# Optimization experiments

Hardware: AMD Instinct MI355X
Metric: run time of the kernel (lower is better)

Reference implementation:

```python
import jax, jax.numpy as jnp
import numpy as np

EPSILON = 0.1
N_ITERS = 5
SCALE = 0.05  # keeps exp(-cdist/epsilon) from underflowing to 0


def setup_inputs() -> dict:
    key = jax.random.key(0)
    k1, k2 = jax.random.split(key)
    P = jax.random.normal(k1, (8192, 64), dtype=jnp.float32) * SCALE
    Q = jax.random.normal(k2, (8192, 64), dtype=jnp.float32) * SCALE
    return {"P": P, "Q": Q}


def _cdist(P, Q):
    # Euclidean pairwise distances via the mm expansion (like torch.cdist p=2)
    sq = (jnp.sum(P * P, axis=-1)[:, None]
          + jnp.sum(Q * Q, axis=-1)[None, :]
          - 2.0 * P @ Q.T)
    return jnp.sqrt(jnp.maximum(sq, 0.0))


def reference(P, Q):
    C = _cdist(P, Q)                      # [N, N]
    K = jnp.exp(-C / EPSILON)             # [N, N]
    D = P.shape[1]
    u = jnp.ones((P.shape[0],), dtype=P.dtype) / D
    for _ in range(N_ITERS):              # small fixed iteration count
        v = 1.0 / (K @ u)                 # [N]
        u = 1.0 / (K @ v)                 # [N]
    plan = u[:, None] * K * v[None, :]    # [N, N]
    return jnp.sum(plan * C)
```

## Files before the change

kernel.cpp:

```cpp
#include <hip/hip_runtime.h>
#include <hip/hip_fp16.h>
#include <stdint.h>

#define NROWS 8192
#define DIM 64
#define EPS 0.1f

typedef float f32x4 __attribute__((ext_vector_type(4)));
typedef short s16x8 __attribute__((ext_vector_type(8)));
typedef _Float16 h2 __attribute__((ext_vector_type(2)));


__device__ __forceinline__ float wave_reduce_add(float v) {
  #pragma unroll
  for (int off = 32; off > 0; off >>= 1) v += __shfl_down(v, off, 64);
  return v;
}

__device__ __forceinline__ uint32_t pack_bf16_trunc(float x, float y) {
  return __builtin_amdgcn_perm(__float_as_uint(y), __float_as_uint(x), 0x07060302u);
}

__device__ __forceinline__ int pi_idx(int i) {
  int r = i & 63;
  int tj = r >> 4, quad = (r >> 2) & 3, e = r & 3;
  return (i & ~63) | (quad * 16 + tj * 4 + e);
}


#if __has_builtin(__builtin_amdgcn_cvt_scalef32_pk_f16_fp4)
#define CVT4H(kd, sel) __builtin_amdgcn_cvt_scalef32_pk_f16_fp4((kd), 1.0f, (sel))
#else
__device__ __forceinline__ h2 cvt4h_fb(uint32_t kd, int sel) {
  uint32_t byt  = (kd >> (sel * 8)) & 0xFFu;
  uint32_t selv = (byt & 0xFu) | ((byt >> 4) << 16);
  uint32_t tb = __builtin_amdgcn_perm(0x46444240u, 0x3E3C3800u, selv);
  uint32_t d  = ((tb & 0xFFu) << 8) | ((tb & 0xFF0000u) << 8);
  return __builtin_bit_cast(h2, d);
}
#define CVT4H(kd, sel) cvt4h_fb((kd), (sel))
#endif

#if __has_builtin(__builtin_amdgcn_cvt_scalef32_pk_fp4_f32)
__device__ __forceinline__ uint32_t enc4(float q0, float q1, float q2, float q3) {
  uint32_t pk = __builtin_amdgcn_cvt_scalef32_pk_fp4_f32(0u, q0, q1, 1.0f, 0);
  pk = __builtin_amdgcn_cvt_scalef32_pk_fp4_f32(pk, q2, q3, 1.0f, 1);
  return pk & 0xFFFFu;
}
#else
__device__ __forceinline__ uint32_t enc1(float q) {
  float c = fminf(floorf(2.f * q + 0.5f), 4.f);
  c += (q > 2.5f) ? 1.f : 0.f;
  c += (q > 3.5f) ? 1.f : 0.f;
  return (uint32_t)c;
}
__device__ __forceinline__ uint32_t enc4(float q0, float q1, float q2, float q3) {
  return enc1(q0) | (enc1(q1) << 4) | (enc1(q2) << 8) | (enc1(q3) << 12);
}
#endif

#if __has_builtin(__builtin_amdgcn_exp2f)
#define EXPD(d) __builtin_amdgcn_exp2f(-14.4269504089f * (d))
#else
#define EXPD(d) __expf(-10.0f * (d))
#endif

#define FP4DOT(kd, xv, acc)                                                          \
  acc = __builtin_amdgcn_fdot2(CVT4H((kd), 0), __builtin_bit_cast(h2, (xv).x), acc, false); \
  acc = __builtin_amdgcn_fdot2(CVT4H((kd), 1), __builtin_bit_cast(h2, (xv).y), acc, false); \
  acc = __builtin_amdgcn_fdot2(CVT4H((kd), 2), __builtin_bit_cast(h2, (xv).z), acc, false); \
  acc = __builtin_amdgcn_fdot2(CVT4H((kd), 3), __builtin_bit_cast(h2, (xv).w), acc, false);

#define FIN1(kd, xd_, sel)                                                           \
  {                                                                                  \
    uint32_t byt  = ((kd) >> ((sel) * 8)) & 0xFFu;                                   \
    uint32_t selv = (byt & 0xFu) | ((byt & 0xF0u) << 12);                            \
    uint32_t hi = __builtin_amdgcn_perm(0x4945423Du, 0x3800B500u, selv);             \
    uint32_t lo = __builtin_amdgcn_perm(0x608C978Cu, 0xDE008C00u, selv);             \
    h2 lut = __builtin_bit_cast(h2, lo | (hi << 8));                                 \
    h2 xp  = __builtin_bit_cast(h2, (xd_));                                          \
    s1b = __builtin_amdgcn_fdot2(CVT4H((kd), (sel)), xp, s1b, false);                \
    t2b = __builtin_amdgcn_fdot2(lut, xp, t2b, false);                               \
  }
#define FINDOT(kd, xv) FIN1(kd, (xv).x, 0) FIN1(kd, (xv).y, 1) FIN1(kd, (xv).z, 2) FIN1(kd, (xv).w, 3)


__global__ __launch_bounds__(256) void rownorm_pack(
    const float* __restrict__ P, const float* __restrict__ Q,
    float* __restrict__ p2, float* __restrict__ q2,
    unsigned short* __restrict__ Pb, unsigned short* __restrict__ Qb) {
  int g = blockIdx.x * 256 + threadIdx.x;
  int row = g >> 3, sub = g & 7;
  const float* X;
  float* out;
  unsigned short* Xb;
  int r;
  float sc;
  if (row < NROWS) { X = P; out = p2; Xb = Pb; r = row; sc = -2.f; }
  else             { X = Q; out = q2; Xb = Qb; r = row - NROWS; sc = 1.f; }
  const float4* X4 = (const float4*)(X + (size_t)r * DIM);
  float4 a0 = X4[sub * 2], a1 = X4[sub * 2 + 1];
  float ss = a0.x * a0.x + a0.y * a0.y + a0.z * a0.z + a0.w * a0.w
           + a1.x * a1.x + a1.y * a1.y + a1.z * a1.z + a1.w * a1.w;
  ss += __shfl_xor(ss, 1, 64);
  ss += __shfl_xor(ss, 2, 64);
  ss += __shfl_xor(ss, 4, 64);
  if (sub == 0) out[r] = ss;
  uint4 pk;
  pk.x = pack_bf16_trunc(sc * a0.x, sc * a0.y);
  pk.y = pack_bf16_trunc(sc * a0.z, sc * a0.w);
  pk.z = pack_bf16_trunc(sc * a1.x, sc * a1.y);
  pk.w = pack_bf16_trunc(sc * a1.z, sc * a1.w);
  *(uint4*)(Xb + (size_t)r * DIM + sub * 8) = pk;
}


struct KgenSmem {
  unsigned char A[128 * 128];
  unsigned char B[256 * 128];
};

__device__ __forceinline__ int swiz_off(int row, int kc) {
  return row * 128 + ((kc ^ (row & 7)) << 4);
}

__global__ __launch_bounds__(512) void kgen_kernel(
    const unsigned short* __restrict__ Pb, const unsigned short* __restrict__ Qb,
    const float* __restrict__ p2, const float* __restrict__ q2,
    unsigned char* __restrict__ K4, unsigned char* __restrict__ scales,
    float* __restrict__ rspart) {
  __shared__ KgenSmem sm;
  const int t  = threadIdx.x;
  const int bi = blockIdx.y * 128;
  const int bj = blockIdx.x * 256;

  {
    const uint4* Pb4 = (const uint4*)(Pb + (size_t)bi * DIM);
    const uint4* Qb4 = (const uint4*)(Qb + (size_t)bj * DIM);
    #pragma unroll
    for (int it = 0; it < 2; ++it) {
      int idx = t + it * 512;
      int row = idx >> 3, kc = idx & 7;
      *(uint4*)(sm.A + swiz_off(row, kc)) = Pb4[row * 8 + kc];
    }
    #pragma unroll
    for (int it = 0; it < 4; ++it) {
      int idx = t + it * 512;
      int row = idx >> 3, kc = idx & 7;
      *(uint4*)(sm.B + swiz_off(row, kc)) = Qb4[row * 8 + kc];
    }
  }
  __syncthreads();

  const int w        = t >> 6;
  const int lane     = t & 63;
  const int quad     = lane >> 4;
  const int m16      = lane & 15;
  const int wave_row = (w >> 2) * 64;
  const int wave_col = (w & 3) * 64;

  float pn[4];
  f32x4 qn[4];
  #pragma unroll
  for (int ti = 0; ti < 4; ++ti) pn[ti] = p2[bi + wave_row + ti * 16 + m16];
  #pragma unroll
  for (int tj = 0; tj < 4; ++tj)
    qn[tj] = *(const f32x4*)&q2[bj + wave_col + tj * 16 + quad * 4];

  f32x4 acc[4][4];
  #pragma unroll
  for (int ti = 0; ti < 4; ++ti)
    #pragma unroll
    for (int tj = 0; tj < 4; ++tj) acc[ti][tj] = qn[tj] + pn[ti];

  #pragma unroll
  for (int kstep = 0; kstep < 2; ++kstep) {
    const int kc = kstep * 4 + quad;
    s16x8 af[4], bf[4];
    #pragma unroll
    for (int ti = 0; ti < 4; ++ti)
      af[ti] = *(const s16x8*)(sm.A + swiz_off(wave_row + ti * 16 + m16, kc));
    #pragma unroll
    for (int tj = 0; tj < 4; ++tj)
      bf[tj] = *(const s16x8*)(sm.B + swiz_off(wave_col + tj * 16 + m16, kc));
    #pragma unroll
    for (int ti = 0; ti < 4; ++ti)
      #pragma unroll
      for (int tj = 0; tj < 4; ++tj)
        acc[ti][tj] = __builtin_amdgcn_mfma_f32_16x16x32_bf16(
            bf[tj], af[ti], acc[ti][tj], 0, 0, 0);
  }

  #pragma unroll
  for (int ti = 0; ti < 4; ++ti) {
    const int row = bi + wave_row + ti * 16 + m16;
    float kv[4][4];
    float mx = 0.f, rs = 0.f;
    #pragma unroll
    for (int tj = 0; tj < 4; ++tj) {
      f32x4 sq = acc[ti][tj];
      kv[tj][0] = EXPD(__builtin_amdgcn_sqrtf(fmaxf(sq.x, 0.f)));
      kv[tj][1] = EXPD(__builtin_amdgcn_sqrtf(fmaxf(sq.y, 0.f)));
      kv[tj][2] = EXPD(__builtin_amdgcn_sqrtf(fmaxf(sq.z, 0.f)));
      kv[tj][3] = EXPD(__builtin_amdgcn_sqrtf(fmaxf(sq.w, 0.f)));
      float mt = fmaxf(fmaxf(kv[tj][0], kv[tj][1]), fmaxf(kv[tj][2], kv[tj][3]));
      mx = fmaxf(mx, mt);
      rs += (kv[tj][0] + kv[tj][1]) + (kv[tj][2] + kv[tj][3]);
    }
    mx = fmaxf(mx, __shfl_xor(mx, 16, 64));
    uint32_t eb = (__float_as_uint(mx) >> 23) - 1u;
    float si = __uint_as_float((254u - eb) << 23);
    uint32_t pk0 = enc4(kv[0][0] * si, kv[0][1] * si, kv[0][2] * si, kv[0][3] * si);
    uint32_t pk1 = enc4(kv[1][0] * si, kv[1][1] * si, kv[1][2] * si, kv[1][3] * si);
    uint32_t pk2 = enc4(kv[2][0] * si, kv[2][1] * si, kv[2][2] * si, kv[2][3] * si);
    uint32_t pk3 = enc4(kv[3][0] * si, kv[3][1] * si, kv[3][2] * si, kv[3][3] * si);
    uint2 st = uint2{pk0 | (pk1 << 16), pk2 | (pk3 << 16)};
    *(uint2*)(K4 + (size_t)row * (NROWS / 2) + ((bj + wave_col) >> 1) + quad * 8) = st;
    uint32_t eb2 = (uint32_t)__shfl_xor((int)eb, 32, 64);
    if (quad == 0) {
      *(unsigned short*)(scales + (size_t)row * 256 + ((bj + wave_col) >> 5)) =
          (unsigned short)((eb & 0xFFu) | ((eb2 & 0xFFu) << 8));
    }
    float v = rs;
    v += __shfl_xor(v, 16, 64);
    v += __shfl_xor(v, 32, 64);
    if (quad == 0)
      rspart[(size_t)(blockIdx.x * 4 + (w & 3)) * NROWS + row] = v;
  }
}

__global__ __launch_bounds__(128) void v1_kernel(const float* __restrict__ rspart,
                                                 unsigned short* __restrict__ vb16) {
  int i = blockIdx.x * 128 + threadIdx.x;
  float s = 0.f;
  #pragma unroll 8
  for (int c = 0; c < 128; ++c) s += rspart[(size_t)c * NROWS + i];
  vb16[pi_idx(i)] = __half_as_ushort(__float2half(64.0f / s));
}


__global__ __launch_bounds__(256) void matvec_fp4(
    const unsigned char* __restrict__ K4, const unsigned char* __restrict__ scales,
    const unsigned short* __restrict__ xin, unsigned short* __restrict__ yout) {
  const int t = threadIdx.x, lane = t & 63, w = t >> 6;
  const int p = w >> 1, h = w & 1;
  const int r0 = blockIdx.x * 4 + p * 2;
  const uint4* krow0 = (const uint4*)(K4 + (size_t)r0 * (NROWS / 2));
  const uint4* krow1 = (const uint4*)(K4 + (size_t)(r0 + 1) * (NROWS / 2));
  const unsigned char* srow0 = scales + (size_t)r0 * 256;
  const unsigned char* srow1 = srow0 + 256;
  const uint4* x4 = (const uint4*)xin;
  const int b0 = h * 128 + lane;
  const int b1 = b0 + 64;

  uint4 xa0 = x4[b0 * 4 + 0], xb0 = x4[b0 * 4 + 1];
  uint4 xc0 = x4[b0 * 4 + 2], xd0 = x4[b0 * 4 + 3];
  uint4 xa1 = x4[b1 * 4 + 0], xb1 = x4[b1 * 4 + 1];
  uint4 xc1 = x4[b1 * 4 + 2], xd1 = x4[b1 * 4 + 3];
  uint4 k00 = krow0[b0], k01 = krow0[b1];
  uint4 k10 = krow1[b0], k11 = krow1[b1];
  float S00 = __uint_as_float((uint32_t)srow0[b0] << 23);
  float S01 = __uint_as_float((uint32_t)srow0[b1] << 23);
  float S10 = __uint_as_float((uint32_t)srow1[b0] << 23);
  float S11 = __uint_as_float((uint32_t)srow1[b1] << 23);

  float a0 = 0.f, a1 = 0.f;
  FP4DOT(k00.x, xa0, a0) FP4DOT(k00.y, xb0, a1)
  FP4DOT(k00.z, xc0, a0) FP4DOT(k00.w, xd0, a1)
  float t0 = S00 * (a0 + a1);
  a0 = 0.f; a1 = 0.f;
  FP4DOT(k01.x, xa1, a0) FP4DOT(k01.y, xb1, a1)
  FP4DOT(k01.z, xc1, a0) FP4DOT(k01.w, xd1, a1)
  t0 = fmaf(S01, a0 + a1, t0);
  a0 = 0.f; a1 = 0.f;
  FP4DOT(k10.x, xa0, a0) FP4DOT(k10.y, xb0, a1)
  FP4DOT(k10.z, xc0, a0) FP4DOT(k10.w, xd0, a1)
  float t1 = S10 * (a0 + a1);
  a0 = 0.f; a1 = 0.f;
  FP4DOT(k11.x, xa1, a0) FP4DOT(k11.y, xb1, a1)
  FP4DOT(k11.z, xc1, a0) FP4DOT(k11.w, xd1, a1)
  t1 = fmaf(S11, a0 + a1, t1);

  t0 = wave_reduce_add(t0);
  t1 = wave_reduce_add(t1);
  __shared__ float sred[4][2];
  if (lane == 0) { sred[w][0] = t0; sred[w][1] = t1; }
  __syncthreads();
  if (t < 4) {
    int pp = t >> 1, j = t & 1;
    float tot = sred[pp * 2 + 0][j] + sred[pp * 2 + 1][j];
    yout[pi_idx(blockIdx.x * 4 + pp * 2 + j)] =
        __half_as_ushort(__float2half(1.0f / tot));
  }
}

__global__ __launch_bounds__(256) void final_fp4(
    const unsigned char* __restrict__ K4, const unsigned char* __restrict__ scales,
    const unsigned short* __restrict__ xin, float* __restrict__ partials) {
  const int t = threadIdx.x, lane = t & 63, w = t >> 6;
  const int p = w >> 1, h = w & 1;
  const int r0 = blockIdx.x * 4 + p * 2;
  const uint4* krow0 = (const uint4*)(K4 + (size_t)r0 * (NROWS / 2));
  const uint4* krow1 = (const uint4*)(K4 + (size_t)(r0 + 1) * (NROWS / 2));
  const unsigned char* srow0 = scales + (size_t)r0 * 256;
  const unsigned char* srow1 = srow0 + 256;
  const uint4* x4 = (const uint4*)xin;
  const int b0 = h * 128 + lane;
  const int b1 = b0 + 64;

  uint4 xa0 = x4[b0 * 4 + 0], xb0 = x4[b0 * 4 + 1];
  uint4 xc0 = x4[b0 * 4 + 2], xd0 = x4[b0 * 4 + 3];
  uint4 xa1 = x4[b1 * 4 + 0], xb1 = x4[b1 * 4 + 1];
  uint4 xc1 = x4[b1 * 4 + 2], xd1 = x4[b1 * 4 + 3];
  uint4 k00 = krow0[b0], k01 = krow0[b1];
  uint4 k10 = krow1[b0], k11 = krow1[b1];
  uint32_t sb00 = srow0[b0], sb01 = srow0[b1];
  uint32_t sb10 = srow1[b0], sb11 = srow1[b1];

  float s1_0, s2_0, s1_1, s2_1;
  {
    float S = __uint_as_float(sb00 << 23);
    float lnS = ((float)(int)sb00 - 127.f) * 0.69314718f;
    float s1b = 0.f, t2b = 0.f;
    FINDOT(k00.x, xa0) FINDOT(k00.y, xb0) FINDOT(k00.z, xc0) FINDOT(k00.w, xd0)
    s1_0 = S * s1b;
    s2_0 = S * fmaf(lnS, s1b, t2b);
  }
  {
    float S = __uint_as_float(sb01 << 23);
    float lnS = ((float)(int)sb01 - 127.f) * 0.69314718f;
    float s1b = 0.f, t2b = 0.f;
    FINDOT(k01.x, xa1) FINDOT(k01.y, xb1) FINDOT(k01.z, xc1) FINDOT(k01.w, xd1)
    s1_0 = fmaf(S, s1b, s1_0);
    s2_0 = fmaf(S, fmaf(lnS, s1b, t2b), s2_0);
  }
  {
    float S = __uint_as_float(sb10 << 23);
    float lnS = ((float)(int)sb10 - 127.f) * 0.69314718f;
    float s1b = 0.f, t2b = 0.f;
    FINDOT(k10.x, xa0) FINDOT(k10.y, xb0) FINDOT(k10.z, xc0) FINDOT(k10.w, xd0)
    s1_1 = S * s1b;
    s2_1 = S * fmaf(lnS, s1b, t2b);
  }
  {
    float S = __uint_as_float(sb11 << 23);
    float lnS = ((float)(int)sb11 - 127.f) * 0.69314718f;
    float s1b = 0.f, t2b = 0.f;
    FINDOT(k11.x, xa1) FINDOT(k11.y, xb1) FINDOT(k11.z, xc1) FINDOT(k11.w, xd1)
    s1_1 = fmaf(S, s1b, s1_1);
    s2_1 = fmaf(S, fmaf(lnS, s1b, t2b), s2_1);
  }

  s1_0 = wave_reduce_add(s1_0);
  s2_0 = wave_reduce_add(s2_0);
  s1_1 = wave_reduce_add(s1_1);
  s2_1 = wave_reduce_add(s2_1);
  __shared__ float sred[4][4];
  if (lane == 0) {
    sred[w][0] = s1_0; sred[w][1] = s2_0; sred[w][2] = s1_1; sred[w][3] = s2_1;
  }
  __syncthreads();
  if (t == 0) {
    float acc = 0.f;
    #pragma unroll
    for (int pp = 0; pp < 2; ++pp)
      #pragma unroll
      for (int j = 0; j < 2; ++j) {
        float s1 = sred[pp * 2 + 0][j * 2 + 0] + sred[pp * 2 + 1][j * 2 + 0];
        float s2 = sred[pp * 2 + 0][j * 2 + 1] + sred[pp * 2 + 1][j * 2 + 1];
        acc += s2 / s1;
      }
    partials[blockIdx.x] = (-EPS) * acc;
  }
}

__global__ __launch_bounds__(256) void reduce_kernel(
    const float* __restrict__ partials, float* __restrict__ out) {
  const int t = threadIdx.x;
  float s = 0.f;
  #pragma unroll
  for (int i = 0; i < 8; ++i) s += partials[t + i * 256];
  s = wave_reduce_add(s);
  __shared__ float red[4];
  int lane = t & 63, wid = t >> 6;
  if (lane == 0) red[wid] = s;
  __syncthreads();
  if (t == 0) out[0] = red[0] + red[1] + red[2] + red[3];
}


extern "C" void kernel_launch(void* const* d_in, const int* in_sizes, int n_in,
                              void* d_out, int out_size, void* d_ws, size_t ws_size,
                              hipStream_t stream) {
  const float* P = (const float*)d_in[0];
  const float* Q = (const float*)d_in[1];
  float* out = (float*)d_out;

  char* ws = (char*)d_ws;
  unsigned char* K4     = (unsigned char*)ws;
  unsigned char* scales = (unsigned char*)(ws + 33554432);
  float* rspart   = (float*)(ws + 35651584);
  float* p2       = (float*)(ws + 39845888);
  float* q2       = (float*)(ws + 39878656);
  float* partials = (float*)(ws + 39911424);
  unsigned short* ub16 = (unsigned short*)(ws + 39919616);
  unsigned short* vb16 = ub16 + NROWS;
  unsigned short* Pb   = (unsigned short*)(ws + 39952384);
  unsigned short* Qb   = (unsigned short*)(ws + 41000960);

  rownorm_pack<<<512, 256, 0, stream>>>(P, Q, p2, q2, Pb, Qb);
  kgen_kernel<<<dim3(NROWS / 256, NROWS / 128), 512, 0, stream>>>(
      Pb, Qb, p2, q2, K4, scales, rspart);
  v1_kernel<<<NROWS / 128, 128, 0, stream>>>(rspart, vb16);

  for (int m = 1; m < 9; ++m) {
    const unsigned short* xin = (m & 1) ? vb16 : ub16;
    unsigned short* yout      = (m & 1) ? ub16 : vb16;
    matvec_fp4<<<NROWS / 4, 256, 0, stream>>>(K4, scales, xin, yout);
  }

  final_fp4<<<NROWS / 4, 256, 0, stream>>>(K4, scales, vb16, partials);
  reduce_kernel<<<1, 256, 0, stream>>>(partials, out);
}
```

Before: 177.9 us.

## Restructure fp4 matvec: four rows per wave with prefetched column chunks

Each wave of the matvec kernel now owns four full rows of K and walks the 256 column blocks in four steps, instead of two waves splitting two rows. The x vector chunk loaded per step is reused across four rows, and the next step's loads are issued before the current step's math (software prefetch). The cross-wave shared-memory reduction and __syncthreads are removed, and the grid shrinks to NROWS/16 blocks. Fewer blocks and more registers per thread may reduce the number of loads in flight across the GPU.

```diff
diff --git a/kernel.cpp b/kernel.cpp
--- a/kernel.cpp
+++ b/kernel.cpp
@@ -243,56 +243,66 @@
     const unsigned char* __restrict__ K4, const unsigned char* __restrict__ scales,
     const unsigned short* __restrict__ xin, unsigned short* __restrict__ yout) {
   const int t = threadIdx.x, lane = t & 63, w = t >> 6;
-  const int p = w >> 1, h = w & 1;
-  const int r0 = blockIdx.x * 4 + p * 2;
-  const uint4* krow0 = (const uint4*)(K4 + (size_t)r0 * (NROWS / 2));
-  const uint4* krow1 = (const uint4*)(K4 + (size_t)(r0 + 1) * (NROWS / 2));
-  const unsigned char* srow0 = scales + (size_t)r0 * 256;
-  const unsigned char* srow1 = srow0 + 256;
+  const int r0 = blockIdx.x * 16 + w * 4;
+  const uint4* kr0 = (const uint4*)(K4 + (size_t)r0 * (NROWS / 2));
+  const uint4* kr1 = (const uint4*)(K4 + (size_t)(r0 + 1) * (NROWS / 2));
+  const uint4* kr2 = (const uint4*)(K4 + (size_t)(r0 + 2) * (NROWS / 2));
+  const uint4* kr3 = (const uint4*)(K4 + (size_t)(r0 + 3) * (NROWS / 2));
+  const unsigned char* sr0 = scales + (size_t)r0 * 256;
+  const unsigned char* sr1 = sr0 + 256;
+  const unsigned char* sr2 = sr0 + 512;
+  const unsigned char* sr3 = sr0 + 768;
   const uint4* x4 = (const uint4*)xin;
-  const int b0 = h * 128 + lane;
-  const int b1 = b0 + 64;
-
-  uint4 xa0 = x4[b0 * 4 + 0], xb0 = x4[b0 * 4 + 1];
-  uint4 xc0 = x4[b0 * 4 + 2], xd0 = x4[b0 * 4 + 3];
-  uint4 xa1 = x4[b1 * 4 + 0], xb1 = x4[b1 * 4 + 1];
-  uint4 xc1 = x4[b1 * 4 + 2], xd1 = x4[b1 * 4 + 3];
-  uint4 k00 = krow0[b0], k01 = krow0[b1];
-  uint4 k10 = krow1[b0], k11 = krow1[b1];
-  float S00 = __uint_as_float((uint32_t)srow0[b0] << 23);
-  float S01 = __uint_as_float((uint32_t)srow0[b1] << 23);
-  float S10 = __uint_as_float((uint32_t)srow1[b0] << 23);
-  float S11 = __uint_as_float((uint32_t)srow1[b1] << 23);
-
-  float a0 = 0.f, a1 = 0.f;
-  FP4DOT(k00.x, xa0, a0) FP4DOT(k00.y, xb0, a1)
-  FP4DOT(k00.z, xc0, a0) FP4DOT(k00.w, xd0, a1)
-  float t0 = S00 * (a0 + a1);
-  a0 = 0.f; a1 = 0.f;
-  FP4DOT(k01.x, xa1, a0) FP4DOT(k01.y, xb1, a1)
-  FP4DOT(k01.z, xc1, a0) FP4DOT(k01.w, xd1, a1)
-  t0 = fmaf(S01, a0 + a1, t0);
-  a0 = 0.f; a1 = 0.f;
-  FP4DOT(k10.x, xa0, a0) FP4DOT(k10.y, xb0, a1)
-  FP4DOT(k10.z, xc0, a0) FP4DOT(k10.w, xd0, a1)
-  float t1 = S10 * (a0 + a1);
-  a0 = 0.f; a1 = 0.f;
-  FP4DOT(k11.x, xa1, a0) FP4DOT(k11.y, xb1, a1)
-  FP4DOT(k11.z, xc1, a0) FP4DOT(k11.w, xd1, a1)
-  t1 = fmaf(S11, a0 + a1, t1);
+
+  int b = lane;
+  uint4 nx0 = x4[b * 4 + 0], nx1 = x4[b * 4 + 1];
+  uint4 nx2 = x4[b * 4 + 2], nx3 = x4[b * 4 + 3];
+  uint4 nk0 = kr0[b], nk1 = kr1[b], nk2 = kr2[b], nk3 = kr3[b];
+
+  float t0 = 0.f, t1 = 0.f, t2 = 0.f, t3 = 0.f;
+  #pragma unroll
+  for (int s = 0; s < 4; ++s) {
+    uint4 cx0 = nx0, cx1 = nx1, cx2 = nx2, cx3 = nx3;
+    uint4 ck0 = nk0, ck1 = nk1, ck2 = nk2, ck3 = nk3;
+    uint32_t sb0 = sr0[b], sb1 = sr1[b], sb2 = sr2[b], sb3 = sr3[b];
+    if (s < 3) {
+      int bn = b + 64;
+      nx0 = x4[bn * 4 + 0]; nx1 = x4[bn * 4 + 1];
+      nx2 = x4[bn * 4 + 2]; nx3 = x4[bn * 4 + 3];
+      nk0 = kr0[bn]; nk1 = kr1[bn]; nk2 = kr2[bn]; nk3 = kr3[bn];
+      b = bn;
+    }
+    float a0, a1;
+    a0 = 0.f; a1 = 0.f;
+    FP4DOT(ck0.x, cx0, a0) FP4DOT(ck0.y, cx1, a1)
+    FP4DOT(ck0.z, cx2, a0) FP4DOT(ck0.w, cx3, a1)
+    t0 = fmaf(__uint_as_float(sb0 << 23), a0 + a1, t0);
+    a0 = 0.f; a1 = 0.f;
+    FP4DOT(ck1.x, cx0, a0) FP4DOT(ck1.y, cx1, a1)
+    FP4DOT(ck1.z, cx2, a0) FP4DOT(ck1.w, cx3, a1)
+    t1 = fmaf(__uint_as_float(sb1 << 23), a0 + a1, t1);
+    a0 = 0.f; a1 = 0.f;
+    FP4DOT(ck2.x, cx0, a0) FP4DOT(ck2.y, cx1, a1)
+    FP4DOT(ck2.z, cx2, a0) FP4DOT(ck2.w, cx3, a1)
+    t2 = fmaf(__uint_as_float(sb2 << 23), a0 + a1, t2);
+    a0 = 0.f; a1 = 0.f;
+    FP4DOT(ck3.x, cx0, a0) FP4DOT(ck3.y, cx1, a1)
+    FP4DOT(ck3.z, cx2, a0) FP4DOT(ck3.w, cx3, a1)
+    t3 = fmaf(__uint_as_float(sb3 << 23), a0 + a1, t3);
+  }
 
   t0 = wave_reduce_add(t0);
   t1 = wave_reduce_add(t1);
-  __shared__ float sred[4][2];
-  if (lane == 0) { sred[w][0] = t0; sred[w][1] = t1; }
-  __syncthreads();
-  if (t < 4) {
-    int pp = t >> 1, j = t & 1;
-    float tot = sred[pp * 2 + 0][j] + sred[pp * 2 + 1][j];
-    yout[pi_idx(blockIdx.x * 4 + pp * 2 + j)] =
-        __half_as_ushort(__float2half(1.0f / tot));
-  }
-}
+  t2 = wave_reduce_add(t2);
+  t3 = wave_reduce_add(t3);
+  if (lane == 0) {
+    yout[pi_idx(r0 + 0)] = __half_as_ushort(__float2half(1.0f / t0));
+    yout[pi_idx(r0 + 1)] = __half_as_ushort(__float2half(1.0f / t1));
+    yout[pi_idx(r0 + 2)] = __half_as_ushort(__float2half(1.0f / t2));
+    yout[pi_idx(r0 + 3)] = __half_as_ushort(__float2half(1.0f / t3));
+  }
+}
+
 
 __global__ __launch_bounds__(256) void final_fp4(
     const unsigned char* __restrict__ K4, const unsigned char* __restrict__ scales,
@@ -416,7 +426,7 @@
   for (int m = 1; m < 9; ++m) {
     const unsigned short* xin = (m & 1) ? vb16 : ub16;
     unsigned short* yout      = (m & 1) ? ub16 : vb16;
-    matvec_fp4<<<NROWS / 4, 256, 0, stream>>>(K4, scales, xin, yout);
+    matvec_fp4<<<NROWS / 16, 256, 0, stream>>>(K4, scales, xin, yout);
   }
 
   final_fp4<<<NROWS / 4, 256, 0, stream>>>(K4, scales, vb16, partials);
```

New measurement: 179.6 us. About the same (+0.9%).
